# Performance work log

Measured on AMD Instinct MI355X. Metric: run time of the kernel, lower is better.

Reference implementation:

```python
import jax, jax.numpy as jnp
import numpy as np

IN_FEATURES = 8192
OUT_FEATURES = 8192
W_BITS = 4
SCALE = float(2 ** 16)


def pbatch_round_quantize(W, n, scale=SCALE):
    """Faithful jnp port of pbatch_round_quantize.

    The torch module decomposes this quantized matrix into bitplanes packed
    into int32 words and accumulates scale_b * (bitplane @ x); the sum of the
    bitplane contributions is exactly (quantized / scale), so we compute that
    directly.
    """
    W_sign = jnp.sign(W)
    W_fixed = jnp.trunc(W * scale)            # (W * scale).astype(int), trunc toward 0
    v = jnp.abs(W_fixed)
    m = jnp.max(v)
    max_place = jnp.maximum(jnp.ceil(jnp.log2(m)) + 1.0, float(n))
    step = jnp.exp2(max_place - n)            # 2 ** (max_place - n)
    # mask = ((1<<max_place)-1) & ~(step-1) == 2**max_place - step
    mask = jnp.exp2(max_place) - step
    # bins[x] = mask - x*step (decreasing, uniformly spaced); centers are midpoints.
    # np.digitize(v, centers) for decreasing centers counts centers > v:
    #   idx = ceil((mask - v)/step - 0.5); then min(len(centers)-1, idx).
    if n == 1:
        # excl_zero: single bin, centers == bins, index always 0
        j = jnp.zeros_like(v)
    else:
        n_centers = 2 ** n - 1
        idx = jnp.ceil((mask - v) / step - 0.5)
        j = jnp.clip(idx, 0.0, float(n_centers - 1))
    rounded = W_sign * (mask - j * step)
    return rounded / scale


def setup_inputs() -> dict:
    key = jax.random.key(0)
    k_in, k_w, k_b = jax.random.split(key, 3)
    input = jax.random.normal(k_in, (IN_FEATURES,), dtype=jnp.float32)
    # reset_parameters: weight = randn(out, in)
    weight = jax.random.normal(k_w, (OUT_FEATURES, IN_FEATURES), dtype=jnp.float32)
    bound = 1.0 / np.sqrt(IN_FEATURES)
    bias = jax.random.uniform(k_b, (OUT_FEATURES,), dtype=jnp.float32,
                              minval=-bound, maxval=bound)
    return {"input": input, "weight": weight, "bias": bias}


def reference(input, weight, bias):
    # A_bits == 32 -> full-precision activations (no activation fixed-point path).
    Wq = pbatch_round_quantize(weight, W_BITS)       # [out, in]
    out = Wq @ input + bias                          # bit-serial GEMV result
    return out.reshape(1, -1)
```

## Files before the change

kernel.cpp:

```cpp
#include <hip/hip_runtime.h>

#define IN_F 8192
#define OUT_F 8192
#define NT 256
#define VPT 8
#define RPB 8
#define NBLK (OUT_F / RPB)

typedef float f32x4 __attribute__((ext_vector_type(4)));


__device__ __forceinline__ float qterm(float w, float xv, float inv_step, float& vmax) {
    float v = truncf(fabsf(w) * 65536.0f);
    vmax = fmaxf(vmax, v);
    float u = v * inv_step;
    float q = floorf(u + 0.5f);
    q = fminf(fmaxf(q, 1.0f), 15.0f);
    q = (w == 0.0f) ? 0.0f : q;
    float t = q * xv;
    return __uint_as_float(__float_as_uint(t) ^ (__float_as_uint(w) & 0x80000000u));
}

__global__ __launch_bounds__(NT, 4) void gemv_spec_kernel(
    const float* __restrict__ W, const float* __restrict__ x,
    const float* __restrict__ bias, float* __restrict__ out,
    unsigned* __restrict__ blkmax) {
    const int t = threadIdx.x;
    const int lane = t & 63, wid = t >> 6;
    const size_t row0 = (size_t)blockIdx.x * RPB;
    const f32x4* __restrict__ x4 = (const f32x4*)x;
    const float inv_step = 1.0f / 65536.0f;

    f32x4 xv[VPT];
#pragma unroll
    for (int k = 0; k < VPT; ++k) xv[k] = x4[t + NT * k];

    __shared__ float    ssum[RPB][NT / 64];
    __shared__ unsigned smax[NT / 64];
    float vmax = 0.0f;

#pragma unroll 2
    for (int j = 0; j < RPB; ++j) {
        const f32x4* __restrict__ Wr = (const f32x4*)(W + (row0 + j) * IN_F);
        f32x4 wv[VPT];
#pragma unroll
        for (int k = 0; k < VPT; ++k) wv[k] = __builtin_nontemporal_load(Wr + t + NT * k);
        float a = 0.0f;
#pragma unroll
        for (int k = 0; k < VPT; ++k) {
            a += qterm(wv[k].x, xv[k].x, inv_step, vmax);
            a += qterm(wv[k].y, xv[k].y, inv_step, vmax);
            a += qterm(wv[k].z, xv[k].z, inv_step, vmax);
            a += qterm(wv[k].w, xv[k].w, inv_step, vmax);
        }
#pragma unroll
        for (int off = 32; off; off >>= 1) a += __shfl_down(a, off);
        if (lane == 0) ssum[j][wid] = a;
    }

#pragma unroll
    for (int off = 32; off; off >>= 1)
        vmax = fmaxf(vmax, __shfl_down(vmax, off));
    if (lane == 0) smax[wid] = __float_as_uint(vmax);
    __syncthreads();

    if (t < RPB) {
        float s = ssum[t][0] + ssum[t][1] + ssum[t][2] + ssum[t][3];
        out[row0 + t] = s + bias[row0 + t];
    }
    if (t == 0)
        blkmax[blockIdx.x] = max(max(smax[0], smax[1]), max(smax[2], smax[3]));
}

__global__ __launch_bounds__(NT, 4) void gemv_fix_kernel(
    const float* __restrict__ W, const float* __restrict__ x,
    const float* __restrict__ bias, float* __restrict__ out,
    const unsigned* __restrict__ blkmax) {
    const int t = threadIdx.x;
    const int lane = t & 63, wid = t >> 6;
    __shared__ unsigned sred[NT / 64];

    uint4 bv = ((const uint4*)blkmax)[t];
    unsigned m = max(max(bv.x, bv.y), max(bv.z, bv.w));
#pragma unroll
    for (int off = 32; off; off >>= 1)
        m = max(m, (unsigned)__shfl_down((int)m, off));
    if (lane == 0) sred[wid] = m;
    __syncthreads();
    m = max(max(sred[0], sred[1]), max(sred[2], sred[3]));
    const unsigned mi = (unsigned)__uint_as_float(m);

    int mp;
    if (mi <= 1u) mp = 1;
    else          mp = 33 - __clz((int)(mi - 1u));
    if (mp < 4) mp = 4;
    if (mp == 20) return;

    const float inv_step = __builtin_ldexpf(1.0f, 4 - mp);
    const float oscale   = __builtin_ldexpf(1.0f, mp - 20);

    const size_t row0 = (size_t)blockIdx.x * RPB;
    const f32x4* __restrict__ x4 = (const f32x4*)x;

    f32x4 xv[VPT];
#pragma unroll
    for (int k = 0; k < VPT; ++k) xv[k] = x4[t + NT * k];

    __shared__ float ssum[RPB][NT / 64];
    float dummy = 0.0f;

#pragma unroll 2
    for (int j = 0; j < RPB; ++j) {
        const f32x4* __restrict__ Wr = (const f32x4*)(W + (row0 + j) * IN_F);
        f32x4 wv[VPT];
#pragma unroll
        for (int k = 0; k < VPT; ++k) wv[k] = __builtin_nontemporal_load(Wr + t + NT * k);
        float a = 0.0f;
#pragma unroll
        for (int k = 0; k < VPT; ++k) {
            a += qterm(wv[k].x, xv[k].x, inv_step, dummy);
            a += qterm(wv[k].y, xv[k].y, inv_step, dummy);
            a += qterm(wv[k].z, xv[k].z, inv_step, dummy);
            a += qterm(wv[k].w, xv[k].w, inv_step, dummy);
        }
#pragma unroll
        for (int off = 32; off; off >>= 1) a += __shfl_down(a, off);
        if (lane == 0) ssum[j][wid] = a;
    }
    __syncthreads();

    if (t < RPB) {
        float s = ssum[t][0] + ssum[t][1] + ssum[t][2] + ssum[t][3];
        out[row0 + t] = s * oscale + bias[row0 + t];
    }
}

extern "C" void kernel_launch(void* const* d_in, const int* in_sizes, int n_in,
                              void* d_out, int out_size, void* d_ws, size_t ws_size,
                              hipStream_t stream) {
    const float* x    = (const float*)d_in[0];
    const float* W    = (const float*)d_in[1];
    const float* bias = (const float*)d_in[2];
    float* out = (float*)d_out;
    unsigned* blkmax = (unsigned*)d_ws;

    gemv_spec_kernel<<<NBLK, NT, 0, stream>>>(W, x, bias, out, blkmax);
    gemv_fix_kernel<<<NBLK, NT, 0, stream>>>(W, x, bias, out, blkmax);
}
```

Measured before the change: 47.13 us.

## Run fallback GEMV kernel as a single block looping over all rows

The fix-up kernel now launches one block that walks all 8192 rows sequentially, with two block-wide barriers per row, instead of 1024 blocks of 8 rows each. The likely aim is to cut launch and early-exit overhead, since this kernel returns immediately whenever the speculative scale matches (mp == 20). When the fallback path is actually taken it becomes massively serialized. Weight loads are also no longer nontemporal or batched.

```diff
diff --git a/kernel.cpp b/kernel.cpp
--- a/kernel.cpp
+++ b/kernel.cpp
@@ -72,7 +72,7 @@
         blkmax[blockIdx.x] = max(max(smax[0], smax[1]), max(smax[2], smax[3]));
 }
 
-__global__ __launch_bounds__(NT, 4) void gemv_fix_kernel(
+__global__ __launch_bounds__(NT) void gemv_fix_kernel(
     const float* __restrict__ W, const float* __restrict__ x,
     const float* __restrict__ bias, float* __restrict__ out,
     const unsigned* __restrict__ blkmax) {
@@ -98,40 +98,32 @@
 
     const float inv_step = __builtin_ldexpf(1.0f, 4 - mp);
     const float oscale   = __builtin_ldexpf(1.0f, mp - 20);
-
-    const size_t row0 = (size_t)blockIdx.x * RPB;
     const f32x4* __restrict__ x4 = (const f32x4*)x;
 
     f32x4 xv[VPT];
 #pragma unroll
     for (int k = 0; k < VPT; ++k) xv[k] = x4[t + NT * k];
 
-    __shared__ float ssum[RPB][NT / 64];
+    __shared__ float ssum[NT / 64];
     float dummy = 0.0f;
 
-#pragma unroll 2
-    for (int j = 0; j < RPB; ++j) {
-        const f32x4* __restrict__ Wr = (const f32x4*)(W + (row0 + j) * IN_F);
-        f32x4 wv[VPT];
-#pragma unroll
-        for (int k = 0; k < VPT; ++k) wv[k] = __builtin_nontemporal_load(Wr + t + NT * k);
+    for (int r = 0; r < OUT_F; ++r) {
+        const f32x4* __restrict__ Wr = (const f32x4*)(W + (size_t)r * IN_F);
         float a = 0.0f;
-#pragma unroll
         for (int k = 0; k < VPT; ++k) {
-            a += qterm(wv[k].x, xv[k].x, inv_step, dummy);
-            a += qterm(wv[k].y, xv[k].y, inv_step, dummy);
-            a += qterm(wv[k].z, xv[k].z, inv_step, dummy);
-            a += qterm(wv[k].w, xv[k].w, inv_step, dummy);
+            f32x4 wv = Wr[t + NT * k];
+            a += qterm(wv.x, xv[k].x, inv_step, dummy);
+            a += qterm(wv.y, xv[k].y, inv_step, dummy);
+            a += qterm(wv.z, xv[k].z, inv_step, dummy);
+            a += qterm(wv.w, xv[k].w, inv_step, dummy);
         }
 #pragma unroll
         for (int off = 32; off; off >>= 1) a += __shfl_down(a, off);
-        if (lane == 0) ssum[j][wid] = a;
-    }
-    __syncthreads();
-
-    if (t < RPB) {
-        float s = ssum[t][0] + ssum[t][1] + ssum[t][2] + ssum[t][3];
-        out[row0 + t] = s * oscale + bias[row0 + t];
+        if (lane == 0) ssum[wid] = a;
+        __syncthreads();
+        if (t == 0)
+            out[r] = (ssum[0] + ssum[1] + ssum[2] + ssum[3]) * oscale + bias[r];
+        __syncthreads();
     }
 }
 
@@ -145,5 +137,5 @@
     unsigned* blkmax = (unsigned*)d_ws;
 
     gemv_spec_kernel<<<NBLK, NT, 0, stream>>>(W, x, bias, out, blkmax);
-    gemv_fix_kernel<<<NBLK, NT, 0, stream>>>(W, x, bias, out, blkmax);
+    gemv_fix_kernel<<<1, NT, 0, stream>>>(W, x, bias, out, blkmax);
 }
```

Result: no change. 46.78 us (-0.7%).
